# Kernel optimization log

Measured on AMD Instinct MI355X. Metric: run time of the kernel, lower is better.

## Reference

```python
import jax, jax.numpy as jnp
import numpy as np

B, T, D, H = 2, 2048, 1024, 16
HD = D // H  # head dim = 64


def setup_inputs() -> dict:
    key = jax.random.key(0)
    ks = jax.random.split(key, 8)
    scale = 0.02
    return {
        "query_states": jax.random.normal(ks[0], (B, T, D), jnp.float32),
        "key_states": jax.random.normal(ks[1], (B, T, D), jnp.float32),
        "query_mask": jnp.ones((B, T), jnp.float32),
        "key_mask": jnp.ones((B, T), jnp.float32),
        "Wq": jax.random.normal(ks[2], (D, D), jnp.float32) * scale,
        "bq": jnp.zeros((D,), jnp.float32),
        "Wk": jax.random.normal(ks[3], (D, D), jnp.float32) * scale,
        "bk": jnp.zeros((D,), jnp.float32),
        "Wv": jax.random.normal(ks[4], (D, D), jnp.float32) * scale,
        "bv": jnp.zeros((D,), jnp.float32),
        "mask_future": 1,
    }


def _split_heads(x):  # [B,T,D] -> [B,H,T,HD]
    return x.reshape(B, T, H, HD).transpose(0, 2, 1, 3)


def reference(query_states, key_states, query_mask, key_mask, Wq, bq, Wk, bk, Wv, bv, mask_future):
    q = _split_heads(query_states @ Wq.T + bq)
    k = _split_heads(key_states @ Wk.T + bk)
    v = _split_heads(key_states @ Wv.T + bv)
    # [B,H,T,T]
    scores = jnp.einsum("bhqd,bhkd->bhqk", q, k) / jnp.sqrt(jnp.float32(HD))
    scores = scores + (1.0 - key_mask)[:, None, None, :] * -10000.0
    if mask_future:
        causal = (1.0 - jnp.tril(jnp.ones((T, T), jnp.float32))) * -10000.0
        scores = scores + causal[None, None, :, :]
    probs = jax.nn.softmax(scores, axis=-1)
    probs = probs * query_mask[:, None, :, None]  # post-softmax query mask
    ctx = jnp.einsum("bhqk,bhkd->bhqd", probs, v)
    return ctx.transpose(0, 2, 1, 3).reshape(B, T, D)
```

## Files before the change

kernel.cpp:

```cpp
#include <hip/hip_runtime.h>
#include <hip/hip_bf16.h>
#include <stdint.h>

typedef __attribute__((ext_vector_type(8))) short short8;
typedef __attribute__((ext_vector_type(4))) short short4_t;
typedef __attribute__((ext_vector_type(4))) float f32x4;

#define B_ 2
#define T_ 2048
#define D_ 1024
#define H_ 16
#define HD_ 64
#define BT_ 4096
#define NKT64 32

#define QSCALE 0.1803368801111601f
#define PEN2 14426.950408889634f

__device__ __forceinline__ unsigned short f2bf(float f) {
    union { float f; uint32_t u; } v; v.f = f;
    uint32_t u = v.u;
    uint32_t r = (u + 0x7fffu + ((u >> 16) & 1u)) >> 16;
    return (unsigned short)r;
}

__device__ __forceinline__ uint32_t cvtpk(float a, float b) {
    union { __hip_bfloat162 h; uint32_t u; } cv;
    cv.h = __float22bfloat162_rn(make_float2(a, b));
    return cv.u;
}

__device__ __forceinline__ void gld16(const void* g, void* l) {
    __builtin_amdgcn_global_load_lds((const __attribute__((address_space(1))) void*)g,
                                     (__attribute__((address_space(3))) void*)l, 16, 0, 0);
}

__device__ __forceinline__ int swz(int x) { return x ^ (((x >> 7) & 7) << 4); }

__global__ __launch_bounds__(256) void cvt2(const float* __restrict__ s0, unsigned short* __restrict__ d0,
                                            const float* __restrict__ s1, unsigned short* __restrict__ d1,
                                            const float* __restrict__ kmask, float* __restrict__ kpen_g,
                                            int n8) {
    int i = blockIdx.x * 256 + threadIdx.x;
    if (blockIdx.y == 2) {
        if (i < B_ * T_) kpen_g[i] = (1.0f - kmask[i]) * -PEN2;
        return;
    }
    const float* src = blockIdx.y ? s1 : s0;
    unsigned short* dst = blockIdx.y ? d1 : d0;
    if (i >= n8) return;
    const float4* s = (const float4*)src + (size_t)i * 2;
    float4 a = s[0], b4 = s[1];
    short8 o;
    o[0] = (short)f2bf(a.x);  o[1] = (short)f2bf(a.y);
    o[2] = (short)f2bf(a.z);  o[3] = (short)f2bf(a.w);
    o[4] = (short)f2bf(b4.x); o[5] = (short)f2bf(b4.y);
    o[6] = (short)f2bf(b4.z); o[7] = (short)f2bf(b4.w);
    *(short8*)(dst + (size_t)i * 8) = o;
}

__global__ __launch_bounds__(256) void cvt3(const float* __restrict__ s0, unsigned short* __restrict__ d0,
                                            const float* __restrict__ s1, unsigned short* __restrict__ d1,
                                            const float* __restrict__ s2, unsigned short* __restrict__ d2,
                                            int n8) {
    const float* src = blockIdx.y == 0 ? s0 : (blockIdx.y == 1 ? s1 : s2);
    unsigned short* dst = blockIdx.y == 0 ? d0 : (blockIdx.y == 1 ? d1 : d2);
    int i = blockIdx.x * 256 + threadIdx.x;
    if (i >= n8) return;
    const float4* s = (const float4*)src + (size_t)i * 2;
    float4 a = s[0], b4 = s[1];
    short8 o;
    o[0] = (short)f2bf(a.x);  o[1] = (short)f2bf(a.y);
    o[2] = (short)f2bf(a.z);  o[3] = (short)f2bf(a.w);
    o[4] = (short)f2bf(b4.x); o[5] = (short)f2bf(b4.y);
    o[6] = (short)f2bf(b4.z); o[7] = (short)f2bf(b4.w);
    *(short8*)(dst + (size_t)i * 8) = o;
}

__global__ __launch_bounds__(256) void qkv_gemm_fused(const unsigned short* __restrict__ xq,
                                                      const unsigned short* __restrict__ xk,
                                                      const unsigned short* __restrict__ wq,
                                                      const unsigned short* __restrict__ wk,
                                                      const unsigned short* __restrict__ wv,
                                                      const float* __restrict__ bq,
                                                      const float* __restrict__ bk,
                                                      const float* __restrict__ bv,
                                                      unsigned short* __restrict__ q_ws,
                                                      unsigned short* __restrict__ k_ws,
                                                      unsigned short* __restrict__ v8_ws) {
    __shared__ unsigned short Al[128 * 32];
    __shared__ unsigned short Bl[128 * 32];
    const int K = D_;
    int z = blockIdx.z;
    const unsigned short* X = (z == 0) ? xq : xk;
    const unsigned short* W = (z == 0) ? wq : (z == 1 ? wk : wv);
    const float* bias = (z == 0) ? bq : (z == 1 ? bk : bv);

    int m0 = blockIdx.x * 128, n0 = blockIdx.y * 128;
    int tid = threadIdx.x, lane = tid & 63, w = tid >> 6;
    int wr = w >> 1, wc = w & 1;

    f32x4 acc[4][4];
#pragma unroll
    for (int i = 0; i < 4; i++)
#pragma unroll
        for (int j = 0; j < 4; j++) acc[i][j] = (f32x4){0.f, 0.f, 0.f, 0.f};

    int srow0 = (lane >> 2);
    int skch = (lane & 3) * 8;

    for (int kt = 0; kt < K / 32; ++kt) {
        int kb = kt * 32;
#pragma unroll
        for (int t = 0; t < 2; ++t) {
            int ins = w * 2 + t;
            int row = ins * 16 + srow0;
            gld16(X + (size_t)(m0 + row) * K + kb + skch, (char*)Al + ins * 1024);
            gld16(W + (size_t)(n0 + row) * K + kb + skch, (char*)Bl + ins * 1024);
        }
        __syncthreads();
        short8 af[4], bf[4];
#pragma unroll
        for (int mi = 0; mi < 4; mi++)
            af[mi] = *(const short8*)(Al + (wr * 64 + mi * 16 + (lane & 15)) * 32 + (lane >> 4) * 8);
#pragma unroll
        for (int ni = 0; ni < 4; ni++)
            bf[ni] = *(const short8*)(Bl + (wc * 64 + ni * 16 + (lane & 15)) * 32 + (lane >> 4) * 8);
#pragma unroll
        for (int mi = 0; mi < 4; mi++)
#pragma unroll
            for (int ni = 0; ni < 4; ni++)
                acc[mi][ni] = __builtin_amdgcn_mfma_f32_16x16x32_bf16(af[mi], bf[ni], acc[mi][ni], 0, 0, 0);
        __syncthreads();
    }

    if (z < 2) {
        unsigned short* outp = (z == 0) ? q_ws : k_ws;
        float osc = (z == 0) ? QSCALE : 1.0f;
#pragma unroll
        for (int ni = 0; ni < 4; ni++) {
            int n = n0 + wc * 64 + ni * 16 + (lane & 15);
            float bv2 = bias[n];
            int h = n >> 6, hd = n & 63;
#pragma unroll
            for (int mi = 0; mi < 4; mi++) {
#pragma unroll
                for (int r = 0; r < 4; r++) {
                    int m = m0 + wr * 64 + mi * 16 + (lane >> 4) * 4 + r;
                    int b = m >> 11, t = m & (T_ - 1);
                    outp[((size_t)(b * H_ + h) * T_ + t) * HD_ + hd] = f2bf((acc[mi][ni][r] + bv2) * osc);
                }
            }
        }
    } else {
#pragma unroll
        for (int ni = 0; ni < 4; ni++) {
            int n = n0 + wc * 64 + ni * 16 + (lane & 15);
            float bv2 = bias[n];
            int h = n >> 6, hd = n & 63;
#pragma unroll
            for (int mi = 0; mi < 4; mi++) {
                int m = m0 + wr * 64 + mi * 16 + (lane >> 4) * 4;
                int b = m >> 11, t = m & (T_ - 1);
                short4_t pk;
#pragma unroll
                for (int r = 0; r < 4; r++) pk[r] = (short)f2bf(acc[mi][ni][r] + bv2);
                *(short4_t*)(v8_ws + (((size_t)(b * H_ + h) * 256 + (t >> 3)) * HD_ + hd) * 8 + (t & 7)) = pk;
            }
        }
    }
}

__global__ __launch_bounds__(256) void attn(const unsigned short* __restrict__ q_ws,
                                            const unsigned short* __restrict__ k_ws,
                                            const unsigned short* __restrict__ v8_ws,
                                            const float* __restrict__ qmask,
                                            const float* __restrict__ kpen_g,
                                            const int* __restrict__ mfp,
                                            float* __restrict__ out) {
    __shared__ char SH[4 * 2048 * 4 + 1024];

    int w = threadIdx.x >> 6;
    int lane = threadIdx.x & 63;
    int lg = lane >> 4, q = lane & 15;
    int bid = blockIdx.x;
    int qt = 63 - (bid >> 5);
    int bh = bid & 31;
    int b = bh >> 4, h = bh & 15;
    int q0 = qt * 32;
    int mf = mfp[0];
    int nkt = mf ? (qt >> 1) + 1 : NKT64;
    char* Pw = SH + w * 4096;

    int base = nkt >> 2, rem = nkt & 3;
    int cnt = base + (w < rem ? 1 : 0);
    int start = w * base + (w < rem ? w : rem);

    short8 qf[2][2];
#pragma unroll
    for (int m = 0; m < 2; m++) {
        const unsigned short* qp = q_ws + ((size_t)bh * T_ + q0 + m * 16 + q) * HD_ + lg * 8;
        qf[m][0] = *(const short8*)qp;
        qf[m][1] = *(const short8*)(qp + 32);
    }

    f32x4 o[2][4];
#pragma unroll
    for (int m = 0; m < 2; m++)
#pragma unroll
        for (int i = 0; i < 4; i++) o[m][i] = (f32x4){0.f, 0.f, 0.f, 0.f};
    float mrow[2] = {-1e30f, -1e30f};
    float lrow[2] = {0.f, 0.f};

    const float* kpenb = kpen_g + b * T_;

    for (int kt = start; kt < start + cnt; ++kt) {
        int kv0 = kt * 64;

        f32x4 s[2][4];
        __builtin_amdgcn_s_setprio(1);
#pragma unroll
        for (int nb = 0; nb < 4; nb++) {
            const unsigned short* kp = k_ws + ((size_t)bh * T_ + kv0 + nb * 16 + q) * HD_ + lg * 8;
            short8 kf0 = *(const short8*)kp;
            short8 kf1 = *(const short8*)(kp + 32);
#pragma unroll
            for (int m = 0; m < 2; m++) {
                f32x4 z = (f32x4){0.f, 0.f, 0.f, 0.f};
                z = __builtin_amdgcn_mfma_f32_16x16x32_bf16(kf0, qf[m][0], z, 0, 0, 0);
                z = __builtin_amdgcn_mfma_f32_16x16x32_bf16(kf1, qf[m][1], z, 0, 0, 0);
                s[m][nb] = z;
            }
        }
        __builtin_amdgcn_s_setprio(0);

        short8 vf[4][2];
        const unsigned short* vbase = v8_ws + (((size_t)bh * 256 + (kv0 >> 3) + lg) * 64 + q) * 8;
#pragma unroll
        for (int nbh = 0; nbh < 4; nbh++) {
            vf[nbh][0] = *(const short8*)(vbase + nbh * 128);
            vf[nbh][1] = *(const short8*)(vbase + nbh * 128 + 2048);
        }

        f32x4 kp4[4];
#pragma unroll
        for (int nb = 0; nb < 4; nb++)
            kp4[nb] = *(const f32x4*)(kpenb + kv0 + nb * 16 + lg * 4);

        bool diag = mf && (kv0 + 63 > q0);
#pragma unroll
        for (int m = 0; m < 2; m++) {
            int qg = q0 + m * 16 + q;
#pragma unroll
            for (int nb = 0; nb < 4; nb++) {
#pragma unroll
                for (int r = 0; r < 4; r++) {
                    float v = s[m][nb][r] + kp4[nb][r];
                    if (diag) {
                        int kvg = kv0 + nb * 16 + lg * 4 + r;
                        v = (kvg > qg) ? v - PEN2 : v;
                    }
                    s[m][nb][r] = v;
                }
            }
            float xm = fmaxf(
                fmaxf(fmaxf(fmaxf(s[m][0][0], s[m][0][1]), fmaxf(s[m][0][2], s[m][0][3])),
                      fmaxf(fmaxf(s[m][1][0], s[m][1][1]), fmaxf(s[m][1][2], s[m][1][3]))),
                fmaxf(fmaxf(fmaxf(s[m][2][0], s[m][2][1]), fmaxf(s[m][2][2], s[m][2][3])),
                      fmaxf(fmaxf(s[m][3][0], s[m][3][1]), fmaxf(s[m][3][2], s[m][3][3]))));
            xm = fmaxf(xm, __shfl_xor(xm, 16));
            xm = fmaxf(xm, __shfl_xor(xm, 32));

            if (__any(xm > mrow[m])) {
                float mn = fmaxf(mrow[m], xm);
                float sc = __builtin_amdgcn_exp2f(mrow[m] - mn);
                mrow[m] = mn;
                lrow[m] *= sc;
#pragma unroll
                for (int nbh = 0; nbh < 4; nbh++)
#pragma unroll
                    for (int r = 0; r < 4; r++) o[m][nbh][r] *= sc;
            }

#pragma unroll
            for (int nb = 0; nb < 4; nb++)
#pragma unroll
                for (int r = 0; r < 4; r++)
                    s[m][nb][r] = __builtin_amdgcn_exp2f(s[m][nb][r] - mrow[m]);

            float rs = ((s[m][0][0] + s[m][0][1]) + (s[m][0][2] + s[m][0][3]))
                     + ((s[m][1][0] + s[m][1][1]) + (s[m][1][2] + s[m][1][3]))
                     + ((s[m][2][0] + s[m][2][1]) + (s[m][2][2] + s[m][2][3]))
                     + ((s[m][3][0] + s[m][3][1]) + (s[m][3][2] + s[m][3][3]));
            rs += __shfl_xor(rs, 16);
            rs += __shfl_xor(rs, 32);
            lrow[m] += rs;

#pragma unroll
            for (int nb = 0; nb < 4; nb++) {
                uint2 ww;
                ww.x = cvtpk(s[m][nb][0], s[m][nb][1]);
                ww.y = cvtpk(s[m][nb][2], s[m][nb][3]);
                *(uint2*)(Pw + m * 2048 + swz(q * 128 + nb * 32 + lg * 8)) = ww;
            }
        }

        short8 pf[2][2];
#pragma unroll
        for (int m = 0; m < 2; m++) {
            pf[m][0] = *(const short8*)(Pw + m * 2048 + swz(q * 128 + lg * 16));
            pf[m][1] = *(const short8*)(Pw + m * 2048 + swz(q * 128 + 64 + lg * 16));
        }

        __builtin_amdgcn_s_setprio(1);
#pragma unroll
        for (int nbh = 0; nbh < 4; nbh++) {
#pragma unroll
            for (int m = 0; m < 2; m++) {
                o[m][nbh] = __builtin_amdgcn_mfma_f32_16x16x32_bf16(vf[nbh][0], pf[m][0], o[m][nbh], 0, 0, 0);
                o[m][nbh] = __builtin_amdgcn_mfma_f32_16x16x32_bf16(vf[nbh][1], pf[m][1], o[m][nbh], 0, 0, 0);
            }
        }
        __builtin_amdgcn_s_setprio(0);
    }

    __syncthreads();
    float* OS = (float*)SH;
    float* ML = (float*)(SH + 32768);
#pragma unroll
    for (int m = 0; m < 2; m++)
#pragma unroll
        for (int nbh = 0; nbh < 4; nbh++)
            *(f32x4*)(OS + w * 2048 + ((m * 4 + nbh) * 64 + lane) * 4) = o[m][nbh];
    if (lane < 16) {
#pragma unroll
        for (int m = 0; m < 2; m++) {
            float2 ml2 = make_float2(mrow[m], lrow[m]);
            *(float2*)(ML + ((w * 2 + m) * 16 + q) * 2) = ml2;
        }
    }
    __syncthreads();

#pragma unroll
    for (int m = 0; m < 2; m++) {
        float2 ml0 = *(const float2*)(ML + ((0 * 2 + m) * 16 + q) * 2);
        float2 ml1 = *(const float2*)(ML + ((1 * 2 + m) * 16 + q) * 2);
        float2 ml2 = *(const float2*)(ML + ((2 * 2 + m) * 16 + q) * 2);
        float2 ml3 = *(const float2*)(ML + ((3 * 2 + m) * 16 + q) * 2);
        float M = fmaxf(fmaxf(ml0.x, ml1.x), fmaxf(ml2.x, ml3.x));
        float e0 = __builtin_amdgcn_exp2f(ml0.x - M), e1 = __builtin_amdgcn_exp2f(ml1.x - M);
        float e2 = __builtin_amdgcn_exp2f(ml2.x - M), e3 = __builtin_amdgcn_exp2f(ml3.x - M);
        float den = ml0.y * e0 + ml1.y * e1 + ml2.y * e2 + ml3.y * e3;

        f32x4 O0 = *(const f32x4*)(OS + 0 * 2048 + ((m * 4 + w) * 64 + lane) * 4);
        f32x4 O1 = *(const f32x4*)(OS + 1 * 2048 + ((m * 4 + w) * 64 + lane) * 4);
        f32x4 O2 = *(const f32x4*)(OS + 2 * 2048 + ((m * 4 + w) * 64 + lane) * 4);
        f32x4 O3 = *(const f32x4*)(OS + 3 * 2048 + ((m * 4 + w) * 64 + lane) * 4);

        int qg = q0 + m * 16 + q;
        float inv = qmask[b * T_ + qg] / den;
        f32x4 ov;
#pragma unroll
        for (int r = 0; r < 4; r++)
            ov[r] = (O0[r] * e0 + O1[r] * e1 + O2[r] * e2 + O3[r] * e3) * inv;
        *(f32x4*)(out + ((size_t)(b * T_ + qg)) * D_ + h * 64 + w * 16 + lg * 4) = ov;
    }
}

extern "C" void kernel_launch(void* const* d_in, const int* in_sizes, int n_in,
                              void* d_out, int out_size, void* d_ws, size_t ws_size,
                              hipStream_t stream) {
    const float* xq = (const float*)d_in[0];
    const float* xk = (const float*)d_in[1];
    const float* qmask = (const float*)d_in[2];
    const float* kmask = (const float*)d_in[3];
    const float* Wq = (const float*)d_in[4];
    const float* bq = (const float*)d_in[5];
    const float* Wk = (const float*)d_in[6];
    const float* bk = (const float*)d_in[7];
    const float* Wv = (const float*)d_in[8];
    const float* bv = (const float*)d_in[9];
    const int* mf = (const int*)d_in[10];
    float* out = (float*)d_out;

    char* ws = (char*)d_ws;
    unsigned short* xq_bf = (unsigned short*)(ws);
    unsigned short* xk_bf = (unsigned short*)(ws + (8u << 20));
    unsigned short* wq_bf = (unsigned short*)(ws + (16u << 20));
    unsigned short* wk_bf = (unsigned short*)(ws + (18u << 20));
    unsigned short* wv_bf = (unsigned short*)(ws + (20u << 20));
    unsigned short* q_ws  = (unsigned short*)(ws + (22u << 20));
    unsigned short* k_ws  = (unsigned short*)(ws + (30u << 20));
    unsigned short* v8_ws = (unsigned short*)(ws + (38u << 20));
    float* kpen_g         = (float*)(ws + (46u << 20));

    cvt2<<<dim3(BT_ * D_ / 8 / 256, 3), 256, 0, stream>>>(xq, xq_bf, xk, xk_bf, kmask, kpen_g, BT_ * D_ / 8);
    cvt3<<<dim3(D_ * D_ / 8 / 256, 3), 256, 0, stream>>>(Wq, wq_bf, Wk, wk_bf, Wv, wv_bf, D_ * D_ / 8);

    dim3 gg(BT_ / 128, D_ / 128, 3);
    qkv_gemm_fused<<<gg, 256, 0, stream>>>(xq_bf, xk_bf, wq_bf, wk_bf, wv_bf, bq, bk, bv,
                                           q_ws, k_ws, v8_ws);

    attn<<<2048, 256, 0, stream>>>(q_ws, k_ws, v8_ws, qmask, kpen_g, mf, out);
}
```

Before: 125.4 us.

## Split attention KV range across two waves instead of four per block

Attention blocks now use 2 waves (128 threads) instead of 4, with KV tiles interleaved between waves (kt = w, w+2, ...) rather than split into contiguous chunks. Shared memory shrinks accordingly, and the final cross-wave softmax merge combines two partials, each wave writing 16 rows × 64 columns. This halves the LDS and merge overhead per block and lets more blocks fit per CU, but each wave processes twice as many KV tiles, which lengthens per-block latency for long causal rows.

```diff
diff --git a/kernel.cpp b/kernel.cpp
--- a/kernel.cpp
+++ b/kernel.cpp
@@ -171,14 +171,14 @@
     }
 }
 
-__global__ __launch_bounds__(256) void attn(const unsigned short* __restrict__ q_ws,
+__global__ __launch_bounds__(128) void attn(const unsigned short* __restrict__ q_ws,
                                             const unsigned short* __restrict__ k_ws,
                                             const unsigned short* __restrict__ v8_ws,
                                             const float* __restrict__ qmask,
                                             const float* __restrict__ kpen_g,
                                             const int* __restrict__ mfp,
                                             float* __restrict__ out) {
-    __shared__ char SH[4 * 2048 * 4 + 1024];
+    __shared__ char SH[16384 + 512];
 
     int w = threadIdx.x >> 6;
     int lane = threadIdx.x & 63;
@@ -192,10 +192,6 @@
     int nkt = mf ? (qt >> 1) + 1 : NKT64;
     char* Pw = SH + w * 4096;
 
-    int base = nkt >> 2, rem = nkt & 3;
-    int cnt = base + (w < rem ? 1 : 0);
-    int start = w * base + (w < rem ? w : rem);
-
     short8 qf[2][2];
 #pragma unroll
     for (int m = 0; m < 2; m++) {
@@ -214,7 +210,7 @@
 
     const float* kpenb = kpen_g + b * T_;
 
-    for (int kt = start; kt < start + cnt; ++kt) {
+    for (int kt = w; kt < nkt; kt += 2) {
         int kv0 = kt * 64;
 
         f32x4 s[2][4];
@@ -326,7 +322,7 @@
 
     __syncthreads();
     float* OS = (float*)SH;
-    float* ML = (float*)(SH + 32768);
+    float* ML = (float*)(SH + 16384);
 #pragma unroll
     for (int m = 0; m < 2; m++)
 #pragma unroll
@@ -341,29 +337,28 @@
     }
     __syncthreads();
 
-#pragma unroll
-    for (int m = 0; m < 2; m++) {
-        float2 ml0 = *(const float2*)(ML + ((0 * 2 + m) * 16 + q) * 2);
-        float2 ml1 = *(const float2*)(ML + ((1 * 2 + m) * 16 + q) * 2);
-        float2 ml2 = *(const float2*)(ML + ((2 * 2 + m) * 16 + q) * 2);
-        float2 ml3 = *(const float2*)(ML + ((3 * 2 + m) * 16 + q) * 2);
-        float M = fmaxf(fmaxf(ml0.x, ml1.x), fmaxf(ml2.x, ml3.x));
-        float e0 = __builtin_amdgcn_exp2f(ml0.x - M), e1 = __builtin_amdgcn_exp2f(ml1.x - M);
-        float e2 = __builtin_amdgcn_exp2f(ml2.x - M), e3 = __builtin_amdgcn_exp2f(ml3.x - M);
-        float den = ml0.y * e0 + ml1.y * e1 + ml2.y * e2 + ml3.y * e3;
-
-        f32x4 O0 = *(const f32x4*)(OS + 0 * 2048 + ((m * 4 + w) * 64 + lane) * 4);
-        f32x4 O1 = *(const f32x4*)(OS + 1 * 2048 + ((m * 4 + w) * 64 + lane) * 4);
-        f32x4 O2 = *(const f32x4*)(OS + 2 * 2048 + ((m * 4 + w) * 64 + lane) * 4);
-        f32x4 O3 = *(const f32x4*)(OS + 3 * 2048 + ((m * 4 + w) * 64 + lane) * 4);
+    {
+        int m = w;
+        float2 mlA = *(const float2*)(ML + ((0 * 2 + m) * 16 + q) * 2);
+        float2 mlB = *(const float2*)(ML + ((1 * 2 + m) * 16 + q) * 2);
+        float M = fmaxf(mlA.x, mlB.x);
+        float eA = __builtin_amdgcn_exp2f(mlA.x - M);
+        float eB = __builtin_amdgcn_exp2f(mlB.x - M);
+        float den = mlA.y * eA + mlB.y * eB;
 
         int qg = q0 + m * 16 + q;
         float inv = qmask[b * T_ + qg] / den;
-        f32x4 ov;
-#pragma unroll
-        for (int r = 0; r < 4; r++)
-            ov[r] = (O0[r] * e0 + O1[r] * e1 + O2[r] * e2 + O3[r] * e3) * inv;
-        *(f32x4*)(out + ((size_t)(b * T_ + qg)) * D_ + h * 64 + w * 16 + lg * 4) = ov;
+        float* op = out + ((size_t)(b * T_ + qg)) * D_ + h * 64 + lg * 4;
+#pragma unroll
+        for (int nbh = 0; nbh < 4; nbh++) {
+            f32x4 OA = *(const f32x4*)(OS + 0 * 2048 + ((m * 4 + nbh) * 64 + lane) * 4);
+            f32x4 OB = *(const f32x4*)(OS + 1 * 2048 + ((m * 4 + nbh) * 64 + lane) * 4);
+            f32x4 ov;
+#pragma unroll
+            for (int r = 0; r < 4; r++)
+                ov[r] = (OA[r] * eA + OB[r] * eB) * inv;
+            *(f32x4*)(op + nbh * 16) = ov;
+        }
     }
 }
 
@@ -401,5 +396,5 @@
     qkv_gemm_fused<<<gg, 256, 0, stream>>>(xq_bf, xk_bf, wq_bf, wk_bf, wv_bf, bq, bk, bv,
                                            q_ws, k_ws, v8_ws);
 
-    attn<<<2048, 256, 0, stream>>>(q_ws, k_ws, v8_ws, qmask, kpen_g, mf, out);
-}
+    attn<<<2048, 128, 0, stream>>>(q_ws, k_ws, v8_ws, qmask, kpen_g, mf, out);
+}
```

Result: faster. 117.7 us (-6.1%).
